# Performance work log

Hardware: AMD Instinct MI355X
Metric: run time of the kernel (lower is better)

## Reference

```python
import jax, jax.numpy as jnp
import numpy as np


def _pos_encoding(seq_length: int, d_model: int, dtype):
    # wave[j] = 10000 ** (j / d_model) for every dim index j (pairs share base exponent pattern)
    j = jnp.arange(d_model, dtype=dtype)
    wave = jnp.power(jnp.asarray(10000.0, dtype), j / d_model)  # [d_model]
    pos = jnp.arange(seq_length, dtype=dtype)                    # [S]
    angles = pos[:, None] / wave[None, :]                        # [S, d_model]
    even = (jnp.arange(d_model) % 2) == 0
    return jnp.where(even[None, :], jnp.sin(angles), jnp.cos(angles))


def setup_inputs() -> dict:
    key = jax.random.key(0)
    x = jax.random.normal(key, (8, 4096, 1024), dtype=jnp.float32)
    return {"x": x}


def reference(x) -> jnp.ndarray:
    B, S, D = x.shape
    pe = _pos_encoding(S, D, x.dtype)  # [S, D], broadcast over batch
    return x + pe[None, :, :]
```

## Files before the change

### kernel.cpp

```cpp
#include <hip/hip_runtime.h>
#include <math.h>

constexpr int B = 8;
constexpr int S = 4096;
constexpr int D = 1024;
constexpr int DQ = D / 4;
constexpr int DQ_SHIFT = 8;
constexpr int PLANE4 = S * DQ;
constexpr int TOTAL4 = B * PLANE4;

#define NEG_L2_10000_OVER_D (-13.287712379549449f / 1024.0f)

__global__ __launch_bounds__(256)
void pe_add_kernel(const float* __restrict__ x, float* __restrict__ out) {
    const int idx4 = blockIdx.x * blockDim.x + threadIdx.x;

    const float4* __restrict__ xv = (const float4*)x;
    float4* __restrict__ ov = (float4*)out;
    float4 v = xv[idx4];

    const int pidx = idx4 & (PLANE4 - 1);
    const int dq   = pidx & (DQ - 1);
    const int s    = pidx >> DQ_SHIFT;
    const int d0   = dq << 2;

    const float fs = (float)s;
    const float a0 = fs * exp2f((float)(d0 + 0) * NEG_L2_10000_OVER_D);
    const float a1 = fs * exp2f((float)(d0 + 1) * NEG_L2_10000_OVER_D);
    const float a2 = fs * exp2f((float)(d0 + 2) * NEG_L2_10000_OVER_D);
    const float a3 = fs * exp2f((float)(d0 + 3) * NEG_L2_10000_OVER_D);

    v.x += __sinf(a0);
    v.y += __cosf(a1);
    v.z += __sinf(a2);
    v.w += __cosf(a3);

    ov[idx4] = v;
}

extern "C" void kernel_launch(void* const* d_in, const int* in_sizes, int n_in,
                              void* d_out, int out_size, void* d_ws, size_t ws_size,
                              hipStream_t stream) {
    const float* x = (const float*)d_in[0];
    float* out = (float*)d_out;

    const int threads = 256;
    const int blocks = TOTAL4 / threads;
    pe_add_kernel<<<blocks, threads, 0, stream>>>(x, out);
}
```

Measured before the change: 219.5 us.

## Compute positional encoding once per position and reuse across batch with nontemporal IO

Each thread now handles one (s, d-quad) position for all 8 batch entries. It computes the sin/cos encoding once and adds it to 8 vectors loaded up front with nontemporal loads, then writes them back with nontemporal stores. This removes redundant transcendental work and gives each thread more loads in flight. In exchange the grid is 8x smaller and each thread uses more registers.

```diff
diff --git a/kernel.cpp b/kernel.cpp
--- a/kernel.cpp
+++ b/kernel.cpp
@@ -7,22 +7,26 @@
 constexpr int DQ = D / 4;
 constexpr int DQ_SHIFT = 8;
 constexpr int PLANE4 = S * DQ;
-constexpr int TOTAL4 = B * PLANE4;
+
+typedef float floatx4 __attribute__((ext_vector_type(4)));
 
 #define NEG_L2_10000_OVER_D (-13.287712379549449f / 1024.0f)
 
 __global__ __launch_bounds__(256)
 void pe_add_kernel(const float* __restrict__ x, float* __restrict__ out) {
-    const int idx4 = blockIdx.x * blockDim.x + threadIdx.x;
+    const int t = blockIdx.x * blockDim.x + threadIdx.x;
 
-    const float4* __restrict__ xv = (const float4*)x;
-    float4* __restrict__ ov = (float4*)out;
-    float4 v = xv[idx4];
+    const floatx4* __restrict__ xv = (const floatx4*)x;
+    floatx4*       __restrict__ ov = (floatx4*)out;
 
-    const int pidx = idx4 & (PLANE4 - 1);
-    const int dq   = pidx & (DQ - 1);
-    const int s    = pidx >> DQ_SHIFT;
-    const int d0   = dq << 2;
+    floatx4 v[B];
+#pragma unroll
+    for (int b = 0; b < B; ++b)
+        v[b] = __builtin_nontemporal_load(&xv[b * PLANE4 + t]);
+
+    const int dq = t & (DQ - 1);
+    const int s  = t >> DQ_SHIFT;
+    const int d0 = dq << 2;
 
     const float fs = (float)s;
     const float a0 = fs * exp2f((float)(d0 + 0) * NEG_L2_10000_OVER_D);
@@ -30,12 +34,20 @@
     const float a2 = fs * exp2f((float)(d0 + 2) * NEG_L2_10000_OVER_D);
     const float a3 = fs * exp2f((float)(d0 + 3) * NEG_L2_10000_OVER_D);
 
-    v.x += __sinf(a0);
-    v.y += __cosf(a1);
-    v.z += __sinf(a2);
-    v.w += __cosf(a3);
+    const float p0 = __sinf(a0);
+    const float p1 = __cosf(a1);
+    const float p2 = __sinf(a2);
+    const float p3 = __cosf(a3);
 
-    ov[idx4] = v;
+#pragma unroll
+    for (int b = 0; b < B; ++b) {
+        floatx4 r = v[b];
+        r.x += p0;
+        r.y += p1;
+        r.z += p2;
+        r.w += p3;
+        __builtin_nontemporal_store(r, &ov[b * PLANE4 + t]);
+    }
 }
 
 extern "C" void kernel_launch(void* const* d_in, const int* in_sizes, int n_in,
@@ -45,6 +57,6 @@
     float* out = (float*)d_out;
 
     const int threads = 256;
-    const int blocks = TOTAL4 / threads;
+    const int blocks = PLANE4 / threads;
     pe_add_kernel<<<blocks, threads, 0, stream>>>(x, out);
 }
```

After: 233.8 us. 6.5% more time.
